# Kernel optimization log

Measured on AMD Instinct MI355X. Metric: run time of the kernel, lower is better.

The kernel has to match this reference:

```python
import jax, jax.numpy as jnp
import numpy as np

SIZE, D, DLOC, NUM_LABELS = 784, 32, 2, 10
LABEL_SITE = SIZE // 2
INIT_STD = 0.01


def tree_contract(mats):
    # mats: [n, B, D, D]; binary-tree pairwise matmul matching the torch loop
    # (odd level: last matrix set aside, re-appended after the pairwise bmm)
    n = mats.shape[0]
    while n > 1:
        if n % 2 == 1:
            lone = mats[-1:]
            mats = mats[:-1]
        else:
            lone = None
        mats = jnp.einsum('nbij,nbjk->nbik', mats[0::2], mats[1::2])
        if lone is not None:
            mats = jnp.concatenate([mats, lone], axis=0)
        n = mats.shape[0]
    return mats[0]  # [B, D, D]


def setup_inputs() -> dict:
    key = jax.random.key(0)
    k1, k2, k3 = jax.random.split(key, 3)
    batch_input = jax.random.uniform(k1, (128, SIZE), dtype=jnp.float32)
    # 'random_eye' init: identity (broadcast over site / physical / label dims) + noise
    core_tensors = (jnp.broadcast_to(jnp.eye(D, dtype=jnp.float32)[None, :, :, None],
                                     (SIZE, D, D, DLOC))
                    + INIT_STD * jax.random.normal(k2, (SIZE, D, D, DLOC), dtype=jnp.float32))
    label_tensor = (jnp.broadcast_to(jnp.eye(D, dtype=jnp.float32)[:, :, None],
                                     (D, D, NUM_LABELS))
                    + INIT_STD * jax.random.normal(k3, (D, D, NUM_LABELS), dtype=jnp.float32))
    return {"batch_input": batch_input, "core_tensors": core_tensors,
            "label_tensor": label_tensor}


def reference(batch_input, core_tensors, label_tensor):
    # embed: x -> [1-x, x], shape [B, S, d]
    embedded = jnp.stack([1.0 - batch_input, batch_input], axis=-1)
    # contract each core with its local feature vector -> [S, B, D, D]
    batch_mats = jnp.einsum('sijd,bsd->sbij', core_tensors, embedded)
    left = tree_contract(batch_mats[:LABEL_SITE])    # [B, D, D]
    right = tree_contract(batch_mats[LABEL_SITE:])   # [B, D, D]
    # trace(left @ label_l @ right) per batch and label -> [B, num_labels]
    scores = jnp.einsum('bij,jkl,bki->bl', left, label_tensor, right)
    return scores
```

## Files before the change

### kernel.cpp

```cpp
#include <hip/hip_runtime.h>
#include <cstddef>


typedef short bfrag __attribute__((ext_vector_type(4)));
typedef float facc  __attribute__((ext_vector_type(4)));

#if !defined(__HIP_DEVICE_COMPILE__)
#define MFMA16(a, b, c) (c)
#elif __has_builtin(__builtin_amdgcn_mfma_f32_16x16x16bf16_1k)
#define MFMA16(a, b, c) __builtin_amdgcn_mfma_f32_16x16x16bf16_1k(a, b, c, 0, 0, 0)
#elif __has_builtin(__builtin_amdgcn_mfma_f32_16x16x16_bf16)
#define MFMA16(a, b, c) __builtin_amdgcn_mfma_f32_16x16x16_bf16(a, b, c, 0, 0, 0)
#else
#error "no 16x16x16 bf16 MFMA builtin on this target"
#endif

#define CORE2B_DWORDS (784 * 1024)

__device__ __forceinline__ short bf16h(float v) {
  unsigned u = __float_as_uint(v) + 0x8000u;
  return (short)(u >> 16);
}

__device__ __forceinline__ bfrag pack4(const facc v) {
  bfrag r;
#pragma unroll
  for (int j = 0; j < 4; ++j) r[j] = bf16h(v[j]);
  return r;
}

__device__ __forceinline__ void split4(const float* v, bfrag& hi, bfrag& lo) {
#pragma unroll
  for (int j = 0; j < 4; ++j) {
    unsigned u = (__float_as_uint(v[j]) + 0x8000u) & 0xFFFF0000u;
    hi[j] = (short)(u >> 16);
    float lf = v[j] - __uint_as_float(u);
    lo[j] = bf16h(lf);
  }
}

__global__ __launch_bounds__(256) void xform_k(const float* __restrict__ core,
                                               unsigned* __restrict__ core2b) {
  const int s = blockIdx.x;
  const int tid = threadIdx.x;
  const int f = tid >> 6;
  const int lane = tid & 63;
  const int col16 = lane & 15;
  const int q = lane >> 4;
  const int r = f >> 1;
  const int h2 = f & 1;
  const int i = 16 * r + col16;
  const int c0 = 16 * h2 + 4 * q;

  const float* src = core + (size_t)s * 2048 + ((size_t)i * 32 + c0) * 2;
  float4 v0 = *(const float4*)(src);
  float4 v1 = *(const float4*)(src + 4);

  unsigned w[4];
  {
    float m0[4] = {v0.x, v0.z, v1.x, v1.z};
    float m1[4] = {v0.y, v0.w, v1.y, v1.w};
#pragma unroll
    for (int j = 0; j < 4; ++j) {
      float e0 = m0[j] - ((i == c0 + j) ? 1.0f : 0.0f);
      float d = m1[j] - m0[j];
      w[j] = ((unsigned)(unsigned short)bf16h(d) << 16) |
             (unsigned)(unsigned short)bf16h(e0);
    }
  }
  *(uint4*)(core2b + (size_t)s * 1024 + (size_t)tid * 4) =
      make_uint4(w[0], w[1], w[2], w[3]);
}

__global__ __launch_bounds__(256, 4) void seg_mfma(const float* __restrict__ x,
                                                   const unsigned* __restrict__ core2b,
                                                   float* __restrict__ seg) {
  const int lane = threadIdx.x & 63;
  const int w = threadIdx.x >> 6;
  const int col16 = lane & 15;
  const int q = lane >> 4;

  const int bid = blockIdx.x;
  const int c2 = bid & 7;
  const int g = (bid >> 3) & 31;
  const int c1 = bid >> 8;
  const int combo = c1 * 8 + c2;
  const int h = combo >> 4;
  const int t = combo & 15;
  const int b = g * 4 + w;

  const int start = (t < 8) ? 25 * t : 200 + 24 * (t - 8);
  const int len = (t < 8) ? 25 : 24;
  const int s_lo = h * 392 + start;
  const int s_hi = s_lo + len - 1;

  facc acc[2][2];
#pragma unroll
  for (int r = 0; r < 2; ++r)
#pragma unroll
    for (int c = 0; c < 2; ++c)
#pragma unroll
      for (int j = 0; j < 4; ++j)
        acc[r][c][j] = (16 * r + 4 * q + j == 16 * c + col16) ? 1.0f : 0.0f;

  const uint4* cp = (const uint4*)core2b;
  const float* xb = x + b * 784;

  for (int s = s_hi; s >= s_lo; --s) {
    uint4 raw[4];
#pragma unroll
    for (int f = 0; f < 4; ++f) raw[f] = cp[(size_t)s * 256 + f * 64 + lane];
    const float xv = xb[s];

    bfrag B[2][2];
#pragma unroll
    for (int h2 = 0; h2 < 2; ++h2)
#pragma unroll
      for (int c = 0; c < 2; ++c) B[h2][c] = pack4(acc[h2][c]);

    bfrag A[2][2];
#pragma unroll
    for (int r = 0; r < 2; ++r)
#pragma unroll
      for (int h2 = 0; h2 < 2; ++h2) {
        unsigned wd[4] = {raw[r * 2 + h2].x, raw[r * 2 + h2].y, raw[r * 2 + h2].z,
                          raw[r * 2 + h2].w};
        bfrag a;
#pragma unroll
        for (int j = 0; j < 4; ++j) {
          float e0 = __uint_as_float(wd[j] << 16);
          float d = __uint_as_float(wd[j] & 0xFFFF0000u);
          a[j] = bf16h(fmaf(xv, d, e0));
        }
        A[r][h2] = a;
      }

#pragma unroll
    for (int r = 0; r < 2; ++r)
#pragma unroll
      for (int c = 0; c < 2; ++c) {
        acc[r][c] = MFMA16(A[r][0], B[0][c], acc[r][c]);
        acc[r][c] = MFMA16(A[r][1], B[1][c], acc[r][c]);
      }
  }

  float4* o = (float4*)(seg + (size_t)((b * 2 + h) * 16 + t) * 1024);
#pragma unroll
  for (int R = 0; R < 2; ++R)
#pragma unroll
    for (int H = 0; H < 2; ++H)
      o[(R * 2 + H) * 64 + lane] =
          make_float4(acc[H][R][0], acc[H][R][1], acc[H][R][2], acc[H][R][3]);
}

__device__ __forceinline__ void fold_step(facc (&acc)[2][2], const float4 (&av)[2][2]) {
  bfrag Ahi[2][2], Alo[2][2], Bhi[2][2], Blo[2][2];
#pragma unroll
  for (int R = 0; R < 2; ++R)
#pragma unroll
    for (int H = 0; H < 2; ++H) {
      float v[4] = {av[R][H].x, av[R][H].y, av[R][H].z, av[R][H].w};
      split4(v, Ahi[R][H], Alo[R][H]);
    }
#pragma unroll
  for (int H = 0; H < 2; ++H)
#pragma unroll
    for (int c = 0; c < 2; ++c) {
      float v[4] = {acc[H][c][0], acc[H][c][1], acc[H][c][2], acc[H][c][3]};
      split4(v, Bhi[H][c], Blo[H][c]);
    }
  facc n[2][2];
#pragma unroll
  for (int R = 0; R < 2; ++R)
#pragma unroll
    for (int c = 0; c < 2; ++c) {
      facc z;
#pragma unroll
      for (int j = 0; j < 4; ++j) z[j] = 0.0f;
#pragma unroll
      for (int H = 0; H < 2; ++H) {
        z = MFMA16(Ahi[R][H], Bhi[H][c], z);
        z = MFMA16(Ahi[R][H], Blo[H][c], z);
        z = MFMA16(Alo[R][H], Bhi[H][c], z);
      }
      n[R][c] = z;
    }
#pragma unroll
  for (int R = 0; R < 2; ++R)
#pragma unroll
    for (int c = 0; c < 2; ++c) acc[R][c] = n[R][c];
}

__global__ __launch_bounds__(256) void finish_k(const float* __restrict__ seg,
                                                const float* __restrict__ label,
                                                float* __restrict__ out) {
  const int tid = threadIdx.x;
  const int lane = tid & 63;
  const int wv = tid >> 6;
  const int side = wv >> 1;
  const int half = wv & 1;
  const int b = blockIdx.x;
  const int chain = 2 * b + side;
  const int col16 = lane & 15;
  const int q = lane >> 4;

  __shared__ float smX[2][32 * 36];
  __shared__ float smF[1024];
  __shared__ float red[40];

  facc acc[2][2];
#pragma unroll
  for (int r = 0; r < 2; ++r)
#pragma unroll
    for (int c = 0; c < 2; ++c)
#pragma unroll
      for (int j = 0; j < 4; ++j)
        acc[r][c][j] = (16 * r + 4 * q + j == 16 * c + col16) ? 1.0f : 0.0f;

  const float* base = seg + (size_t)(chain * 16) * 1024;
  const int t0 = half * 8;

  float4 av[2][2];
#pragma unroll
  for (int R = 0; R < 2; ++R)
#pragma unroll
    for (int H = 0; H < 2; ++H)
      av[R][H] = *(const float4*)&base[(size_t)t0 * 1024 + ((R * 2 + H) * 64 + lane) * 4];
  for (int t = t0; t < t0 + 7; ++t) {
    float4 nav[2][2];
#pragma unroll
    for (int R = 0; R < 2; ++R)
#pragma unroll
      for (int H = 0; H < 2; ++H)
        nav[R][H] =
            *(const float4*)&base[(size_t)(t + 1) * 1024 + ((R * 2 + H) * 64 + lane) * 4];
    fold_step(acc, av);
#pragma unroll
    for (int R = 0; R < 2; ++R)
#pragma unroll
      for (int H = 0; H < 2; ++H) av[R][H] = nav[R][H];
  }
  fold_step(acc, av);

  if (half == 1) {
#pragma unroll
    for (int r = 0; r < 2; ++r)
#pragma unroll
      for (int c = 0; c < 2; ++c)
#pragma unroll
        for (int j = 0; j < 4; ++j)
          smX[side][(16 * r + 4 * q + j) * 36 + 16 * c + col16] = acc[r][c][j];
  }
  __syncthreads();
  if (half == 0) {
    float4 qv[2][2];
#pragma unroll
    for (int R = 0; R < 2; ++R)
#pragma unroll
      for (int H = 0; H < 2; ++H)
        qv[R][H] = *(const float4*)&smX[side][(16 * R + col16) * 36 + 16 * H + 4 * q];
    fold_step(acc, qv);
  }
  __syncthreads();

  if (wv == 0) {
#pragma unroll
    for (int r = 0; r < 2; ++r)
#pragma unroll
      for (int c = 0; c < 2; ++c)
#pragma unroll
        for (int j = 0; j < 4; ++j)
          smX[0][(16 * r + 4 * q + j) * 36 + 16 * c + col16] = acc[r][c][j];
  }
  __syncthreads();
  if (wv == 2) {
    float4 qv[2][2];
#pragma unroll
    for (int R = 0; R < 2; ++R)
#pragma unroll
      for (int H = 0; H < 2; ++H)
        qv[R][H] = *(const float4*)&smX[0][(16 * R + col16) * 36 + 16 * H + 4 * q];
    fold_step(acc, qv);
#pragma unroll
    for (int r = 0; r < 2; ++r)
#pragma unroll
      for (int c = 0; c < 2; ++c)
#pragma unroll
        for (int j = 0; j < 4; ++j)
          smF[(16 * r + 4 * q + j) * 32 + 16 * c + col16] = acc[r][c][j];
  }
  __syncthreads();

  float part[10];
#pragma unroll
  for (int l = 0; l < 10; ++l) part[l] = 0.0f;
#pragma unroll
  for (int u = 0; u < 4; ++u) {
    int e = tid + 256 * u;
    float v = smF[e];
    const float* lb = label + (size_t)e * 10;
#pragma unroll
    for (int l = 0; l < 10; ++l) part[l] += v * lb[l];
  }
#pragma unroll
  for (int l = 0; l < 10; ++l) {
#pragma unroll
    for (int o = 32; o > 0; o >>= 1) part[l] += __shfl_xor(part[l], o, 64);
  }
  if (lane == 0) {
#pragma unroll
    for (int l = 0; l < 10; ++l) red[wv * 10 + l] = part[l];
  }
  __syncthreads();
  if (tid < 10) {
    float s = 0.0f;
#pragma unroll
    for (int v = 0; v < 4; ++v) s += red[v * 10 + tid];
    out[b * 10 + tid] = s;
  }
}

extern "C" void kernel_launch(void* const* d_in, const int* in_sizes, int n_in,
                              void* d_out, int out_size, void* d_ws, size_t ws_size,
                              hipStream_t stream) {
  const float* x = (const float*)d_in[0];
  const float* core = (const float*)d_in[1];
  const float* label = (const float*)d_in[2];
  float* out = (float*)d_out;

  unsigned* core2b = (unsigned*)d_ws;
  float* seg = (float*)d_ws + CORE2B_DWORDS;

  hipLaunchKernelGGL(xform_k, dim3(784), dim3(256), 0, stream, core, core2b);
  hipLaunchKernelGGL(seg_mfma, dim3(1024), dim3(256), 0, stream, x, core2b, seg);
  hipLaunchKernelGGL(finish_k, dim3(128), dim3(256), 0, stream, seg, label, out);
}
```

Before: 95.74 us.

## Fuse segment chain products with in-block tree reduction and use packed bf16 conversion

Result: faster. 93.25 us (-2.6%).

```diff
diff --git a/kernel.cpp b/kernel.cpp
--- a/kernel.cpp
+++ b/kernel.cpp
@@ -22,11 +22,23 @@
   return (short)(u >> 16);
 }
 
+#if defined(__HIP_DEVICE_COMPILE__) && __has_builtin(__builtin_amdgcn_cvt_pk_bf16_f32)
+typedef __bf16 bf16x2 __attribute__((ext_vector_type(2)));
+__device__ __forceinline__ bfrag packf4(float a, float b, float c, float d) {
+  bf16x2 lo = __builtin_amdgcn_cvt_pk_bf16_f32(a, b);
+  bf16x2 hi = __builtin_amdgcn_cvt_pk_bf16_f32(c, d);
+  uint2 u = make_uint2(__builtin_bit_cast(unsigned, lo), __builtin_bit_cast(unsigned, hi));
+  return __builtin_bit_cast(bfrag, u);
+}
+#else
+__device__ __forceinline__ bfrag packf4(float a, float b, float c, float d) {
+  bfrag r; r[0] = bf16h(a); r[1] = bf16h(b); r[2] = bf16h(c); r[3] = bf16h(d);
+  return r;
+}
+#endif
+
 __device__ __forceinline__ bfrag pack4(const facc v) {
-  bfrag r;
-#pragma unroll
-  for (int j = 0; j < 4; ++j) r[j] = bf16h(v[j]);
-  return r;
+  return packf4(v[0], v[1], v[2], v[3]);
 }
 
 __device__ __forceinline__ void split4(const float* v, bfrag& hi, bfrag& lo) {
@@ -37,120 +49,6 @@
     float lf = v[j] - __uint_as_float(u);
     lo[j] = bf16h(lf);
   }
-}
-
-__global__ __launch_bounds__(256) void xform_k(const float* __restrict__ core,
-                                               unsigned* __restrict__ core2b) {
-  const int s = blockIdx.x;
-  const int tid = threadIdx.x;
-  const int f = tid >> 6;
-  const int lane = tid & 63;
-  const int col16 = lane & 15;
-  const int q = lane >> 4;
-  const int r = f >> 1;
-  const int h2 = f & 1;
-  const int i = 16 * r + col16;
-  const int c0 = 16 * h2 + 4 * q;
-
-  const float* src = core + (size_t)s * 2048 + ((size_t)i * 32 + c0) * 2;
-  float4 v0 = *(const float4*)(src);
-  float4 v1 = *(const float4*)(src + 4);
-
-  unsigned w[4];
-  {
-    float m0[4] = {v0.x, v0.z, v1.x, v1.z};
-    float m1[4] = {v0.y, v0.w, v1.y, v1.w};
-#pragma unroll
-    for (int j = 0; j < 4; ++j) {
-      float e0 = m0[j] - ((i == c0 + j) ? 1.0f : 0.0f);
-      float d = m1[j] - m0[j];
-      w[j] = ((unsigned)(unsigned short)bf16h(d) << 16) |
-             (unsigned)(unsigned short)bf16h(e0);
-    }
-  }
-  *(uint4*)(core2b + (size_t)s * 1024 + (size_t)tid * 4) =
-      make_uint4(w[0], w[1], w[2], w[3]);
-}
-
-__global__ __launch_bounds__(256, 4) void seg_mfma(const float* __restrict__ x,
-                                                   const unsigned* __restrict__ core2b,
-                                                   float* __restrict__ seg) {
-  const int lane = threadIdx.x & 63;
-  const int w = threadIdx.x >> 6;
-  const int col16 = lane & 15;
-  const int q = lane >> 4;
-
-  const int bid = blockIdx.x;
-  const int c2 = bid & 7;
-  const int g = (bid >> 3) & 31;
-  const int c1 = bid >> 8;
-  const int combo = c1 * 8 + c2;
-  const int h = combo >> 4;
-  const int t = combo & 15;
-  const int b = g * 4 + w;
-
-  const int start = (t < 8) ? 25 * t : 200 + 24 * (t - 8);
-  const int len = (t < 8) ? 25 : 24;
-  const int s_lo = h * 392 + start;
-  const int s_hi = s_lo + len - 1;
-
-  facc acc[2][2];
-#pragma unroll
-  for (int r = 0; r < 2; ++r)
-#pragma unroll
-    for (int c = 0; c < 2; ++c)
-#pragma unroll
-      for (int j = 0; j < 4; ++j)
-        acc[r][c][j] = (16 * r + 4 * q + j == 16 * c + col16) ? 1.0f : 0.0f;
-
-  const uint4* cp = (const uint4*)core2b;
-  const float* xb = x + b * 784;
-
-  for (int s = s_hi; s >= s_lo; --s) {
-    uint4 raw[4];
-#pragma unroll
-    for (int f = 0; f < 4; ++f) raw[f] = cp[(size_t)s * 256 + f * 64 + lane];
-    const float xv = xb[s];
-
-    bfrag B[2][2];
-#pragma unroll
-    for (int h2 = 0; h2 < 2; ++h2)
-#pragma unroll
-      for (int c = 0; c < 2; ++c) B[h2][c] = pack4(acc[h2][c]);
-
-    bfrag A[2][2];
-#pragma unroll
-    for (int r = 0; r < 2; ++r)
-#pragma unroll
-      for (int h2 = 0; h2 < 2; ++h2) {
-        unsigned wd[4] = {raw[r * 2 + h2].x, raw[r * 2 + h2].y, raw[r * 2 + h2].z,
-                          raw[r * 2 + h2].w};
-        bfrag a;
-#pragma unroll
-        for (int j = 0; j < 4; ++j) {
-          float e0 = __uint_as_float(wd[j] << 16);
-          float d = __uint_as_float(wd[j] & 0xFFFF0000u);
-          a[j] = bf16h(fmaf(xv, d, e0));
-        }
-        A[r][h2] = a;
-      }
-
-#pragma unroll
-    for (int r = 0; r < 2; ++r)
-#pragma unroll
-      for (int c = 0; c < 2; ++c) {
-        acc[r][c] = MFMA16(A[r][0], B[0][c], acc[r][c]);
-        acc[r][c] = MFMA16(A[r][1], B[1][c], acc[r][c]);
-      }
-  }
-
-  float4* o = (float4*)(seg + (size_t)((b * 2 + h) * 16 + t) * 1024);
-#pragma unroll
-  for (int R = 0; R < 2; ++R)
-#pragma unroll
-    for (int H = 0; H < 2; ++H)
-      o[(R * 2 + H) * 64 + lane] =
-          make_float4(acc[H][R][0], acc[H][R][1], acc[H][R][2], acc[H][R][3]);
 }
 
 __device__ __forceinline__ void fold_step(facc (&acc)[2][2], const float4 (&av)[2][2]) {
@@ -191,22 +89,54 @@
     for (int c = 0; c < 2; ++c) acc[R][c] = n[R][c];
 }
 
-__global__ __launch_bounds__(256) void finish_k(const float* __restrict__ seg,
-                                                const float* __restrict__ label,
-                                                float* __restrict__ out) {
+__global__ __launch_bounds__(256) void xform_k(const float* __restrict__ core,
+                                               unsigned* __restrict__ core2b) {
+  const int s = blockIdx.x;
+  const int tid = threadIdx.x;
+  const float4* src = (const float4*)(core + (size_t)s * 2048);
+  unsigned* dst = core2b + (size_t)s * 1024;
+#pragma unroll
+  for (int u = 0; u < 2; ++u) {
+    int v = tid + 256 * u;
+    float4 f = src[v];
+    int i = v >> 4;
+    int c = (v & 15) * 2;
+    int r = i >> 4, col16 = i & 15;
+    int h2 = c >> 4, cl = c & 15;
+    int q = cl >> 2, j = cl & 3;
+    float e0a = f.x - ((i == c) ? 1.0f : 0.0f);
+    float e0b = f.z - ((i == c + 1) ? 1.0f : 0.0f);
+    unsigned wa = ((unsigned)(unsigned short)bf16h(f.y - f.x) << 16) |
+                  (unsigned)(unsigned short)bf16h(e0a);
+    unsigned wb = ((unsigned)(unsigned short)bf16h(f.w - f.z) << 16) |
+                  (unsigned)(unsigned short)bf16h(e0b);
+    int idx = ((r * 2 + h2) * 64 + 16 * q + col16) * 4 + j;
+    *(uint2*)(dst + idx) = make_uint2(wa, wb);
+  }
+}
+
+__global__ __launch_bounds__(512, 4) void kchain(const float* __restrict__ x,
+                                                 const unsigned* __restrict__ core2b,
+                                                 float* __restrict__ halfbuf) {
   const int tid = threadIdx.x;
   const int lane = tid & 63;
-  const int wv = tid >> 6;
-  const int side = wv >> 1;
-  const int half = wv & 1;
-  const int b = blockIdx.x;
-  const int chain = 2 * b + side;
+  const int k = tid >> 6;
   const int col16 = lane & 15;
   const int q = lane >> 4;
 
-  __shared__ float smX[2][32 * 36];
-  __shared__ float smF[1024];
-  __shared__ float red[40];
+  const int bid = blockIdx.x;
+  const int chain = bid >> 1;
+  const int half = bid & 1;
+  const int b = chain >> 1;
+  const int hside = chain & 1;
+
+  const int t = half * 8 + k;
+  const int start = (t < 8) ? 25 * t : 200 + 24 * (t - 8);
+  const int len = (t < 8) ? 25 : 24;
+  const int s_lo = hside * 392 + start;
+  const int s_hi = s_lo + len - 1;
+
+  __shared__ float smX[8][32 * 36];
 
   facc acc[2][2];
 #pragma unroll
@@ -217,86 +147,180 @@
       for (int j = 0; j < 4; ++j)
         acc[r][c][j] = (16 * r + 4 * q + j == 16 * c + col16) ? 1.0f : 0.0f;
 
-  const float* base = seg + (size_t)(chain * 16) * 1024;
-  const int t0 = half * 8;
-
-  float4 av[2][2];
-#pragma unroll
-  for (int R = 0; R < 2; ++R)
-#pragma unroll
-    for (int H = 0; H < 2; ++H)
-      av[R][H] = *(const float4*)&base[(size_t)t0 * 1024 + ((R * 2 + H) * 64 + lane) * 4];
-  for (int t = t0; t < t0 + 7; ++t) {
-    float4 nav[2][2];
-#pragma unroll
-    for (int R = 0; R < 2; ++R)
-#pragma unroll
-      for (int H = 0; H < 2; ++H)
-        nav[R][H] =
-            *(const float4*)&base[(size_t)(t + 1) * 1024 + ((R * 2 + H) * 64 + lane) * 4];
+  const uint4* cp = (const uint4*)core2b;
+  const float* xb = x + b * 784;
+
+  for (int s = s_hi; s >= s_lo; --s) {
+    uint4 raw[4];
+#pragma unroll
+    for (int f = 0; f < 4; ++f) raw[f] = cp[(size_t)s * 256 + f * 64 + lane];
+    const float xv = xb[s];
+
+    bfrag B[2][2];
+#pragma unroll
+    for (int h2 = 0; h2 < 2; ++h2)
+#pragma unroll
+      for (int c = 0; c < 2; ++c) B[h2][c] = pack4(acc[h2][c]);
+
+    bfrag A[2][2];
+#pragma unroll
+    for (int r = 0; r < 2; ++r)
+#pragma unroll
+      for (int h2 = 0; h2 < 2; ++h2) {
+        unsigned wd[4] = {raw[r * 2 + h2].x, raw[r * 2 + h2].y, raw[r * 2 + h2].z,
+                          raw[r * 2 + h2].w};
+        float e[4];
+#pragma unroll
+        for (int j = 0; j < 4; ++j) {
+          float e0 = __uint_as_float(wd[j] << 16);
+          float d = __uint_as_float(wd[j] & 0xFFFF0000u);
+          e[j] = fmaf(xv, d, e0);
+        }
+        A[r][h2] = packf4(e[0], e[1], e[2], e[3]);
+      }
+
+#pragma unroll
+    for (int r = 0; r < 2; ++r)
+#pragma unroll
+      for (int c = 0; c < 2; ++c) {
+        acc[r][c] = MFMA16(A[r][0], B[0][c], acc[r][c]);
+        acc[r][c] = MFMA16(A[r][1], B[1][c], acc[r][c]);
+      }
+  }
+
+#pragma unroll
+  for (int r = 0; r < 2; ++r)
+#pragma unroll
+    for (int c = 0; c < 2; ++c)
+      *(float4*)&smX[k][(16 * c + col16) * 36 + 16 * r + 4 * q] =
+          make_float4(acc[r][c][0], acc[r][c][1], acc[r][c][2], acc[r][c][3]);
+  __syncthreads();
+
+  facc a2[2][2];
+#pragma unroll
+  for (int r = 0; r < 2; ++r)
+#pragma unroll
+    for (int c = 0; c < 2; ++c)
+#pragma unroll
+      for (int j = 0; j < 4; ++j)
+        a2[r][c][j] = (16 * r + 4 * q + j == 16 * c + col16) ? 1.0f : 0.0f;
+
+  const int fo0 = (16 * 0 + col16) * 36 + 4 * q;
+  const int fo1 = (16 * 1 + col16) * 36 + 4 * q;
+
+  if ((k & 1) == 0) {
+    float4 av[2][2];
+#pragma unroll
+    for (int R = 0; R < 2; ++R)
+#pragma unroll
+      for (int H = 0; H < 2; ++H)
+        av[R][H] = *(const float4*)&smX[k][(R ? fo1 : fo0) + 16 * H];
+    fold_step(a2, av);
+#pragma unroll
+    for (int R = 0; R < 2; ++R)
+#pragma unroll
+      for (int H = 0; H < 2; ++H)
+        av[R][H] = *(const float4*)&smX[k + 1][(R ? fo1 : fo0) + 16 * H];
+    fold_step(a2, av);
+  }
+  __syncthreads();
+  if (k == 2 || k == 6) {
+#pragma unroll
+    for (int r = 0; r < 2; ++r)
+#pragma unroll
+      for (int c = 0; c < 2; ++c)
+#pragma unroll
+        for (int j = 0; j < 4; ++j)
+          smX[k][(16 * r + 4 * q + j) * 36 + 16 * c + col16] = a2[r][c][j];
+  }
+  __syncthreads();
+  if (k == 0 || k == 4) {
+    float4 av[2][2];
+#pragma unroll
+    for (int R = 0; R < 2; ++R)
+#pragma unroll
+      for (int H = 0; H < 2; ++H)
+        av[R][H] = *(const float4*)&smX[k + 2][(R ? fo1 : fo0) + 16 * H];
+    fold_step(a2, av);
+  }
+  __syncthreads();
+  if (k == 4) {
+#pragma unroll
+    for (int r = 0; r < 2; ++r)
+#pragma unroll
+      for (int c = 0; c < 2; ++c)
+#pragma unroll
+        for (int j = 0; j < 4; ++j)
+          smX[4][(16 * r + 4 * q + j) * 36 + 16 * c + col16] = a2[r][c][j];
+  }
+  __syncthreads();
+  if (k == 0) {
+    float4 av[2][2];
+#pragma unroll
+    for (int R = 0; R < 2; ++R)
+#pragma unroll
+      for (int H = 0; H < 2; ++H)
+        av[R][H] = *(const float4*)&smX[4][(R ? fo1 : fo0) + 16 * H];
+    fold_step(a2, av);
+    float* rm = halfbuf + (size_t)bid * 1024;
+#pragma unroll
+    for (int r = 0; r < 2; ++r)
+#pragma unroll
+      for (int c = 0; c < 2; ++c)
+#pragma unroll
+        for (int j = 0; j < 4; ++j)
+          rm[(16 * r + 4 * q + j) * 32 + 16 * c + col16] = a2[r][c][j];
+  }
+}
+
+__global__ __launch_bounds__(64) void gfin(const float* __restrict__ halfbuf,
+                                           const float* __restrict__ label,
+                                           float* __restrict__ out) {
+  const int lane = threadIdx.x;
+  const int b = blockIdx.x;
+  const int col16 = lane & 15;
+  const int q = lane >> 4;
+
+  __shared__ float smF[1024];
+
+  facc acc[2][2];
+#pragma unroll
+  for (int r = 0; r < 2; ++r)
+#pragma unroll
+    for (int c = 0; c < 2; ++c)
+#pragma unroll
+      for (int j = 0; j < 4; ++j)
+        acc[r][c][j] = (16 * r + 4 * q + j == 16 * c + col16) ? 1.0f : 0.0f;
+
+  const int slots[4] = {(2 * b + 1) * 2 + 0, (2 * b + 1) * 2 + 1,
+                        (2 * b) * 2 + 0, (2 * b) * 2 + 1};
+#pragma unroll
+  for (int m = 0; m < 4; ++m) {
+    const float* rm = halfbuf + (size_t)slots[m] * 1024;
+    float4 av[2][2];
+#pragma unroll
+    for (int R = 0; R < 2; ++R)
+#pragma unroll
+      for (int H = 0; H < 2; ++H)
+        av[R][H] = *(const float4*)&rm[(16 * R + col16) * 32 + 16 * H + 4 * q];
     fold_step(acc, av);
-#pragma unroll
-    for (int R = 0; R < 2; ++R)
-#pragma unroll
-      for (int H = 0; H < 2; ++H) av[R][H] = nav[R][H];
-  }
-  fold_step(acc, av);
-
-  if (half == 1) {
-#pragma unroll
-    for (int r = 0; r < 2; ++r)
-#pragma unroll
-      for (int c = 0; c < 2; ++c)
-#pragma unroll
-        for (int j = 0; j < 4; ++j)
-          smX[side][(16 * r + 4 * q + j) * 36 + 16 * c + col16] = acc[r][c][j];
-  }
-  __syncthreads();
-  if (half == 0) {
-    float4 qv[2][2];
-#pragma unroll
-    for (int R = 0; R < 2; ++R)
-#pragma unroll
-      for (int H = 0; H < 2; ++H)
-        qv[R][H] = *(const float4*)&smX[side][(16 * R + col16) * 36 + 16 * H + 4 * q];
-    fold_step(acc, qv);
-  }
-  __syncthreads();
-
-  if (wv == 0) {
-#pragma unroll
-    for (int r = 0; r < 2; ++r)
-#pragma unroll
-      for (int c = 0; c < 2; ++c)
-#pragma unroll
-        for (int j = 0; j < 4; ++j)
-          smX[0][(16 * r + 4 * q + j) * 36 + 16 * c + col16] = acc[r][c][j];
-  }
-  __syncthreads();
-  if (wv == 2) {
-    float4 qv[2][2];
-#pragma unroll
-    for (int R = 0; R < 2; ++R)
-#pragma unroll
-      for (int H = 0; H < 2; ++H)
-        qv[R][H] = *(const float4*)&smX[0][(16 * R + col16) * 36 + 16 * H + 4 * q];
-    fold_step(acc, qv);
-#pragma unroll
-    for (int r = 0; r < 2; ++r)
-#pragma unroll
-      for (int c = 0; c < 2; ++c)
-#pragma unroll
-        for (int j = 0; j < 4; ++j)
-          smF[(16 * r + 4 * q + j) * 32 + 16 * c + col16] = acc[r][c][j];
-  }
+  }
+
+#pragma unroll
+  for (int r = 0; r < 2; ++r)
+#pragma unroll
+    for (int c = 0; c < 2; ++c)
+#pragma unroll
+      for (int j = 0; j < 4; ++j)
+        smF[(16 * r + 4 * q + j) * 32 + 16 * c + col16] = acc[r][c][j];
   __syncthreads();
 
   float part[10];
 #pragma unroll
   for (int l = 0; l < 10; ++l) part[l] = 0.0f;
 #pragma unroll
-  for (int u = 0; u < 4; ++u) {
-    int e = tid + 256 * u;
+  for (int u = 0; u < 16; ++u) {
+    int e = lane + 64 * u;
     float v = smF[e];
     const float* lb = label + (size_t)e * 10;
 #pragma unroll
@@ -309,14 +333,7 @@
   }
   if (lane == 0) {
 #pragma unroll
-    for (int l = 0; l < 10; ++l) red[wv * 10 + l] = part[l];
-  }
-  __syncthreads();
-  if (tid < 10) {
-    float s = 0.0f;
-#pragma unroll
-    for (int v = 0; v < 4; ++v) s += red[v * 10 + tid];
-    out[b * 10 + tid] = s;
+    for (int l = 0; l < 10; ++l) out[b * 10 + l] = part[l];
   }
 }
 
@@ -329,9 +346,9 @@
   float* out = (float*)d_out;
 
   unsigned* core2b = (unsigned*)d_ws;
-  float* seg = (float*)d_ws + CORE2B_DWORDS;
+  float* halfbuf = (float*)d_ws + CORE2B_DWORDS;
 
   hipLaunchKernelGGL(xform_k, dim3(784), dim3(256), 0, stream, core, core2b);
-  hipLaunchKernelGGL(seg_mfma, dim3(1024), dim3(256), 0, stream, x, core2b, seg);
-  hipLaunchKernelGGL(finish_k, dim3(128), dim3(256), 0, stream, seg, label, out);
-}
+  hipLaunchKernelGGL(kchain, dim3(512), dim3(512), 0, stream, x, core2b, halfbuf);
+  hipLaunchKernelGGL(gfin, dim3(128), dim3(64), 0, stream, halfbuf, label, out);
+}
```
